# Performance work log

Measured on AMD Instinct MI355X. Metric: run time of the kernel, lower is better.

Reference implementation:

```python
import jax, jax.numpy as jnp
import numpy as np

# Model dims (see init_kwargs)
B, S, H = 1, 1024, 2048
NH, NKV, HD = 16, 4, 128       # query heads, kv heads (GQA), head dim
RD = 64                        # partial rotary dim
E, TOPK, I = 8, 2, 1024        # experts, top-k, expert intermediate
EPS = 1e-6
THETA = 1000000.0


def setup_inputs() -> dict:
    key = jax.random.key(0)
    ks = jax.random.split(key, 12)
    s = 0.02  # init scale
    return {
        "hidden_states": jax.random.normal(ks[0], (B, S, H), jnp.float32),
        "position_ids": jnp.tile(jnp.arange(S, dtype=jnp.int32), (B, 1)),
        "ln1_w": jnp.ones((H,), jnp.float32),
        "q_norm_w": jnp.ones((NH * HD,), jnp.float32),
        "k_norm_w": jnp.ones((NKV * HD,), jnp.float32),
        "wq": jax.random.normal(ks[1], (H, NH * HD), jnp.float32) * s,
        "wk": jax.random.normal(ks[2], (H, NKV * HD), jnp.float32) * s,
        "wv": jax.random.normal(ks[3], (H, NKV * HD), jnp.float32) * s,
        "wo": jax.random.normal(ks[4], (NH * HD, H), jnp.float32) * s,
        "ln2_w": jnp.ones((H,), jnp.float32),
        "router_w": jax.random.normal(ks[5], (H, E), jnp.float32) * s,
        "router_bias": jax.random.normal(ks[6], (E,), jnp.float32) * 0.1,
        "w_gate": jax.random.normal(ks[7], (E, H, I), jnp.float32) * s,
        "w_up": jax.random.normal(ks[8], (E, H, I), jnp.float32) * s,
        "w_down": jax.random.normal(ks[9], (E, I, H), jnp.float32) * s,
    }


def rmsnorm(x, w):
    # fp32 RMSNorm over full last dim (matches DistributedRMSNorm with tp=1)
    xf = x.astype(jnp.float32)
    r = jax.lax.rsqrt(jnp.mean(xf * xf, axis=-1, keepdims=True) + EPS)
    return (xf * r * w).astype(x.dtype)


def _rope(x, cos, sin):
    # partial rotary: only first RD dims of each head are rotated
    xr, xp = x[..., :RD], x[..., RD:]
    half = RD // 2
    rot = jnp.concatenate([-xr[..., half:], xr[..., :half]], axis=-1)
    return jnp.concatenate([xr * cos + rot * sin, xp], axis=-1)


def reference(hidden_states, position_ids, ln1_w, q_norm_w, k_norm_w,
              wq, wk, wv, wo, ln2_w, router_w, router_bias,
              w_gate, w_up, w_down):
    x = hidden_states
    # --- attention block ---
    h = rmsnorm(x, ln1_w)
    Q = h @ wq  # [B,S,NH*HD]
    K = h @ wk  # [B,S,NKV*HD]
    V = h @ wv
    # MiniMax M2 qk_norm: RMSNorm over FULL projection output BEFORE head reshape
    Q = rmsnorm(Q, q_norm_w)
    K = rmsnorm(K, k_norm_w)
    q = Q.reshape(B, S, NH, HD).transpose(0, 2, 1, 3)   # [B,NH,S,HD]
    k = K.reshape(B, S, NKV, HD).transpose(0, 2, 1, 3)  # [B,NKV,S,HD]
    v = V.reshape(B, S, NKV, HD).transpose(0, 2, 1, 3)
    # partial RoPE
    inv = 1.0 / (THETA ** (jnp.arange(0, RD, 2, dtype=jnp.float32) / RD))
    ang = position_ids.astype(jnp.float32)[:, :, None] * inv  # [B,S,RD/2]
    cos = jnp.concatenate([jnp.cos(ang)] * 2, axis=-1)[:, None]  # [B,1,S,RD]
    sin = jnp.concatenate([jnp.sin(ang)] * 2, axis=-1)[:, None]
    q = _rope(q, cos, sin)
    k = _rope(k, cos, sin)
    # GQA expand
    rep = NH // NKV
    k = jnp.repeat(k, rep, axis=1)
    v = jnp.repeat(v, rep, axis=1)
    scores = jnp.einsum('bhqd,bhkd->bhqk', q, k).astype(jnp.float32) / np.sqrt(HD).astype(np.float32)
    causal = jnp.tril(jnp.ones((S, S), bool))
    scores = jnp.where(causal, scores, jnp.float32(-1e30))
    attn = jax.nn.softmax(scores, axis=-1).astype(v.dtype)
    ctx = jnp.einsum('bhqk,bhkd->bhqd', attn, v)
    attn_out = ctx.transpose(0, 2, 1, 3).reshape(B, S, NH * HD) @ wo
    res = x + attn_out
    # --- MoE block ---
    h2 = rmsnorm(res, ln2_w)
    t = h2.reshape(B * S, H)
    logits = t.astype(jnp.float32) @ router_w        # [T,E]
    sc = jax.nn.sigmoid(logits)
    # top-k chosen on bias-corrected scores; weights from uncorrected scores
    _, ti = jax.lax.top_k(sc + router_bias, TOPK)    # [T,TOPK]
    aff = jnp.take_along_axis(sc, ti, axis=-1)
    aff = aff / jnp.sum(aff, axis=-1, keepdims=True)  # normalize_top_k_affinities
    T = B * S
    combine = jnp.zeros((T, E), jnp.float32).at[jnp.arange(T)[:, None], ti].add(aff)
    # SwiGLU experts (dense-compute, sparse-combine reference for blockwise grouped GEMM)
    g = jnp.einsum('th,ehi->tei', t, w_gate)
    u = jnp.einsum('th,ehi->tei', t, w_up)
    act = jax.nn.silu(g) * u
    eo = jnp.einsum('tei,eih->teh', act, w_down)
    moe = jnp.einsum('te,teh->th', combine.astype(eo.dtype), eo)
    return res + moe.reshape(B, S, H)
```

## Files before the change

### kernel.cpp

```cpp
#include <hip/hip_runtime.h>
#include <hip/hip_bf16.h>
#include <cstdint>

static constexpr int S   = 1024;
static constexpr int H   = 2048;
static constexpr int NH  = 16;
static constexpr int NKV = 4;
static constexpr int HD  = 128;
static constexpr int EXPN = 8;
static constexpr int FFI = 1024;

typedef __bf16 bf16x8 __attribute__((ext_vector_type(8)));
typedef float  f32x4  __attribute__((ext_vector_type(4)));
typedef unsigned short ushortx8 __attribute__((ext_vector_type(8)));

#define DEVI __device__ __forceinline__

DEVI unsigned short f2bf(float f) {
    union { float f; uint32_t u; } v; v.f = f;
    uint32_t r = (v.u + 0x7FFFu + ((v.u >> 16) & 1u)) >> 16;
    return (unsigned short)r;
}
DEVI float bf2f(unsigned short s) {
    union { uint32_t u; float f; } v; v.u = ((uint32_t)s) << 16; return v.f;
}

DEVI void atomAdd(float* p, float v) { unsafeAtomicAdd(p, v); }

DEVI void gll16(const unsigned short* g, unsigned short* l) {
    __builtin_amdgcn_global_load_lds(
        (const __attribute__((address_space(1))) unsigned int*)(g),
        (__attribute__((address_space(3))) unsigned int*)(l),
        16, 0, 0);
}

template<int N> DEVI void waitvm() {
    if constexpr (N == 0)      asm volatile("s_waitcnt vmcnt(0)" ::: "memory");
    else if constexpr (N == 2) asm volatile("s_waitcnt vmcnt(2)" ::: "memory");
    else if constexpr (N == 4) asm volatile("s_waitcnt vmcnt(4)" ::: "memory");
    else if constexpr (N == 6) asm volatile("s_waitcnt vmcnt(6)" ::: "memory");
    else static_assert(N == 0 || N == 2 || N == 4 || N == 6, "unsupported vmcnt");
}
DEVI void pipe_barrier() {
    __builtin_amdgcn_sched_barrier(0);
    __builtin_amdgcn_s_barrier();
    __builtin_amdgcn_sched_barrier(0);
}

__global__ __launch_bounds__(256) void transT(const float* __restrict__ in,
                                              unsigned short* __restrict__ outp,
                                              int R, int C)
{
    __shared__ unsigned short tl[64][72];
    int zb = blockIdx.z;
    in   += (size_t)zb * R * C;
    outp += (size_t)zb * R * C;
    int c0 = blockIdx.x * 64, r0 = blockIdx.y * 64;
    int t = threadIdx.x;
    int cq = (t & 15) * 4;
    int rr = t >> 4;
    #pragma unroll
    for (int p = 0; p < 4; ++p) {
        int row = rr + p * 16;
        float4 v = *(const float4*)&in[(size_t)(r0 + row) * C + c0 + cq];
        tl[cq + 0][row] = f2bf(v.x);
        tl[cq + 1][row] = f2bf(v.y);
        tl[cq + 2][row] = f2bf(v.z);
        tl[cq + 3][row] = f2bf(v.w);
    }
    __syncthreads();
    int r8 = (t & 7) * 8;
    int cc = t >> 3;
    #pragma unroll
    for (int p = 0; p < 2; ++p) {
        int col = cc + p * 32;
        ushortx8 v = *(const ushortx8*)&tl[col][r8];
        *(ushortx8*)&outp[(size_t)(c0 + col) * R + r0 + r8] = v;
    }
}

enum { CFG_PROJ3 = 0, CFG_WO = 1, CFG_SCORES = 2, CFG_PV = 3, CFG_GATEUP = 4, CFG_DOWN = 5 };

template<int CFG, int WM, int NI>
__global__ __launch_bounds__(256, 2) void gemm_k(
    const unsigned short* __restrict__ A,
    const unsigned short* __restrict__ B0,
    const unsigned short* __restrict__ B1,
    const unsigned short* __restrict__ B2,
    float* __restrict__ C0,
    float* __restrict__ C1,
    float* __restrict__ C2,
    unsigned short* __restrict__ Cb,
    const float* __restrict__ X,
    const int* __restrict__ cnt,
    const int* __restrict__ tokList,
    int arg0)
{
    constexpr bool DUAL = (CFG == CFG_GATEUP);
    constexpr int BM = WM * 32;
    constexpr int BN = NI * 32;
    constexpr int ASZ = BM * 64;
    constexpr int BSZ = BN * 64;
    constexpr int LD = WM + NI + (DUAL ? NI : 0);

    const int tid = threadIdx.x;
    const int m0 = blockIdx.y * BM;
    int n0 = blockIdx.x * BN;

    int M = S;
    int kbeg = 0, kend = 0, LDA = 0, LDBK = 0, LDC = 0;
    const unsigned short* Ap = A;
    const unsigned short* Bb = B0;
    const unsigned short* Bb2 = B1;
    const int* tlist = nullptr;
    float* Cout = C0;
    int head = 0, e = 0, hl = 0;

    if constexpr (CFG == CFG_PROJ3) {
        int xt = blockIdx.x;
        if (xt < 16)      { Bb = B0; Cout = C0; LDC = 2048; n0 = xt * 128; }
        else if (xt < 20) { Bb = B1; Cout = C1; LDC = 512;  n0 = (xt - 16) * 128; }
        else              { Bb = B2; Cout = C2; LDC = 512;  n0 = (xt - 20) * 128; }
        LDA = H; LDBK = H; kend = H;
    } else if constexpr (CFG == CFG_WO) {
        LDA = H; LDBK = H; LDC = H; kend = H;
    } else if constexpr (CFG == CFG_SCORES) {
        hl = blockIdx.z; head = arg0 + hl;
        if (n0 >= m0 + BM) return;
        Ap = A + (size_t)head * S * HD;
        Bb = B0 + (size_t)(head >> 2) * S * HD;
        kend = HD; LDA = HD; LDBK = HD;
    } else if constexpr (CFG == CFG_PV) {
        int z = blockIdx.z; hl = z >> 2; int ks = z & 3;
        head = arg0 + hl;
        int kcap = m0 + BM;
        kbeg = ks * 256;
        if (kbeg >= kcap) return;
        kend = (kbeg + 256 < kcap) ? kbeg + 256 : kcap;
        Ap = A + (size_t)hl * S * S;
        Bb = B0 + (size_t)(head >> 2) * HD * S;
        LDA = S; LDBK = S;
    } else if constexpr (CFG == CFG_GATEUP) {
        e = blockIdx.z;
        M = cnt[e]; if (m0 >= M) return;
        tlist = tokList + e * S;
        Bb  = B0 + (size_t)e * FFI * H;
        Bb2 = B1 + (size_t)e * FFI * H;
        kend = H; LDA = H; LDBK = H;
    } else {
        e = blockIdx.z;
        M = cnt[e]; if (m0 >= M) return;
        Ap = A + (size_t)e * S * FFI;
        Bb = B0 + (size_t)e * H * FFI;
        kend = FFI; LDA = FFI; LDBK = FFI;
    }

    __shared__ unsigned short As[3 * ASZ];
    __shared__ unsigned short Bs[3 * BSZ];
    __shared__ unsigned short Bs2[DUAL ? 3 * BSZ : 8];

    const int lane = tid & 63, grp = lane >> 4, r16 = lane & 15;
    const int wid = tid >> 6, wr = wid >> 1, wc = wid & 1;
    const int wbase8 = (tid & 0xFFC0) * 8;

    size_t aoff[WM];
    #pragma unroll
    for (int c = 0; c < WM; ++c) {
        int chunk = c * 256 + tid;
        int row = chunk >> 3;
        int kcs = (chunk & 7) * 8;
        int grow = m0 + row;
        if constexpr (CFG == CFG_GATEUP) { int r2 = grow < M ? grow : M - 1; grow = tlist[r2]; }
        else if constexpr (CFG == CFG_DOWN) { grow = grow < M ? grow : M - 1; }
        aoff[c] = (size_t)grow * LDA + (kcs ^ ((row & 7) << 3));
    }
    size_t boff[NI];
    #pragma unroll
    for (int c = 0; c < NI; ++c) {
        int chunk = c * 256 + tid;
        int row = chunk >> 3;
        int kcs = (chunk & 7) * 8;
        boff[c] = (size_t)(n0 + row) * LDBK + (kcs ^ ((row & 7) << 3));
    }

    auto STAGE = [&](int buf, int k0) {
        #pragma unroll
        for (int c = 0; c < WM; ++c)
            gll16(Ap + aoff[c] + k0, &As[buf * ASZ + c * 2048 + wbase8]);
        #pragma unroll
        for (int c = 0; c < NI; ++c)
            gll16(Bb + boff[c] + k0, &Bs[buf * BSZ + c * 2048 + wbase8]);
        if constexpr (DUAL) {
            #pragma unroll
            for (int c = 0; c < NI; ++c)
                gll16(Bb2 + boff[c] + k0, &Bs2[buf * BSZ + c * 2048 + wbase8]);
        }
    };

    f32x4 acc[WM][NI] = {};
    f32x4 acc2[DUAL ? WM : 1][DUAL ? NI : 1] = {};

    auto COMPUTE = [&](int buf) {
        #pragma unroll
        for (int kk = 0; kk < 64; kk += 32) {
            bf16x8 af[WM], bfr[NI], bfr2[DUAL ? NI : 1];
            #pragma unroll
            for (int mi = 0; mi < WM; ++mi) {
                int r = wr * (WM * 16) + mi * 16 + r16;
                int idx = buf * ASZ + r * 64 + ((kk + grp * 8) ^ ((r & 7) << 3));
                af[mi] = __builtin_bit_cast(bf16x8, *(const ushortx8*)&As[idx]);
            }
            #pragma unroll
            for (int ni = 0; ni < NI; ++ni) {
                int r = wc * (NI * 16) + ni * 16 + r16;
                int idx = buf * BSZ + r * 64 + ((kk + grp * 8) ^ ((r & 7) << 3));
                bfr[ni] = __builtin_bit_cast(bf16x8, *(const ushortx8*)&Bs[idx]);
                if constexpr (DUAL)
                    bfr2[ni] = __builtin_bit_cast(bf16x8, *(const ushortx8*)&Bs2[idx]);
            }
            #pragma unroll
            for (int mi = 0; mi < WM; ++mi)
                #pragma unroll
                for (int ni = 0; ni < NI; ++ni) {
                    acc[mi][ni] = __builtin_amdgcn_mfma_f32_16x16x32_bf16(af[mi], bfr[ni], acc[mi][ni], 0, 0, 0);
                    if constexpr (DUAL)
                        acc2[mi][ni] = __builtin_amdgcn_mfma_f32_16x16x32_bf16(af[mi], bfr2[ni], acc2[mi][ni], 0, 0, 0);
                }
        }
    };

    const int nk = (kend - kbeg) >> 6;

    STAGE(0, kbeg);
    if (nk > 1) STAGE(1, kbeg + 64);
    if (nk > 1) waitvm<LD>(); else waitvm<0>();
    pipe_barrier();

    int cur = 0, stg = 2;
    for (int i = 0; i < nk; ++i) {
        if (i + 2 < nk) {
            STAGE(stg, kbeg + (i + 2) * 64);
            stg = (stg == 2) ? 0 : stg + 1;
        }
        COMPUTE(cur);
        cur = (cur == 2) ? 0 : cur + 1;
        if (i + 1 < nk) {
            if (i + 2 < nk) waitvm<LD>();
            else            waitvm<0>();
            pipe_barrier();
        }
    }

    #pragma unroll
    for (int mi = 0; mi < WM; ++mi) {
        #pragma unroll
        for (int ni = 0; ni < NI; ++ni) {
            f32x4 v = acc[mi][ni];
            int col = n0 + wc * (NI * 16) + ni * 16 + r16;
            #pragma unroll
            for (int j = 0; j < 4; ++j) {
                int row = m0 + wr * (WM * 16) + mi * 16 + grp * 4 + j;
                float val = v[j];
                if constexpr (CFG == CFG_PROJ3) {
                    Cout[(size_t)row * LDC + col] = val;
                } else if constexpr (CFG == CFG_WO) {
                    C0[(size_t)row * H + col] = val + X[(size_t)row * H + col];
                } else if constexpr (CFG == CFG_SCORES) {
                    float sv = val * 0.08838834764831845f;
                    if (col > row) sv = -1e30f;
                    C0[((size_t)hl * S + row) * S + col] = sv;
                } else if constexpr (CFG == CFG_PV) {
                    atomAdd(&C0[(size_t)row * 2048 + head * HD + col], val);
                } else if constexpr (CFG == CFG_GATEUP) {
                    if (row < M) {
                        float g = val, u = acc2[mi][ni][j];
                        float a = g / (1.f + expf(-g)) * u;
                        Cb[((size_t)e * S + row) * FFI + col] = f2bf(a);
                    }
                } else {
                    if (row < M) {
                        Cb[((size_t)e * S + row) * H + col] = f2bf(val);
                    }
                }
            }
        }
    }
}

__global__ __launch_bounds__(256) void rms_h(const float* __restrict__ x,
                                             const float* __restrict__ w,
                                             unsigned short* __restrict__ out)
{
    int row = blockIdx.x, tid = threadIdx.x;
    const float* xr = x + (size_t)row * H;
    float4 a = *(const float4*)&xr[tid * 8];
    float4 b = *(const float4*)&xr[tid * 8 + 4];
    float vals[8] = { a.x, a.y, a.z, a.w, b.x, b.y, b.z, b.w };
    float ss = 0;
    #pragma unroll
    for (int j = 0; j < 8; ++j) ss += vals[j] * vals[j];
    __shared__ float red[4];
    #pragma unroll
    for (int o = 32; o; o >>= 1) ss += __shfl_down(ss, o);
    if ((tid & 63) == 0) red[tid >> 6] = ss;
    __syncthreads();
    float tot = red[0] + red[1] + red[2] + red[3];
    float r = rsqrtf(tot * (1.f / H) + 1e-6f);
    ushortx8 ov;
    #pragma unroll
    for (int j = 0; j < 8; ++j) ov[j] = f2bf(vals[j] * r * w[tid * 8 + j]);
    *(ushortx8*)&out[(size_t)row * H + tid * 8] = ov;
}

__global__ __launch_bounds__(256) void qnorm_rope(const float* __restrict__ qbuf,
                                                  const float* __restrict__ qw,
                                                  const int* __restrict__ pos,
                                                  unsigned short* __restrict__ qatt)
{
    int tok = blockIdx.x, tid = threadIdx.x;
    __shared__ float sh[2048];
    __shared__ float red[4];
    const float* xr = qbuf + (size_t)tok * 2048;
    float4 a = *(const float4*)&xr[tid * 8];
    float4 b = *(const float4*)&xr[tid * 8 + 4];
    *(float4*)&sh[tid * 8] = a;
    *(float4*)&sh[tid * 8 + 4] = b;
    float ss = a.x*a.x + a.y*a.y + a.z*a.z + a.w*a.w + b.x*b.x + b.y*b.y + b.z*b.z + b.w*b.w;
    #pragma unroll
    for (int o = 32; o; o >>= 1) ss += __shfl_down(ss, o);
    if ((tid & 63) == 0) red[tid >> 6] = ss;
    __syncthreads();
    float tot = red[0] + red[1] + red[2] + red[3];
    float r = rsqrtf(tot * (1.f / 2048.f) + 1e-6f);
    float p = (float)pos[tok];
    #pragma unroll
    for (int j = 0; j < 8; ++j) {
        int idx = tid * 8 + j;
        int d = idx & 127, hh = idx >> 7;
        float v = sh[idx] * r * qw[idx];
        float o;
        if (d < 64) {
            int jj = d & 31;
            float ang = p * expf((float)jj * -0.43173470268f);
            float c = cosf(ang), sn = sinf(ang);
            if (d < 32) { float v2 = sh[idx + 32] * r * qw[idx + 32]; o = v * c - v2 * sn; }
            else        { float v2 = sh[idx - 32] * r * qw[idx - 32]; o = v * c + v2 * sn; }
        } else o = v;
        qatt[((size_t)hh * S + tok) * HD + d] = f2bf(o);
    }
}

__global__ __launch_bounds__(256) void knorm_rope(const float* __restrict__ kbuf,
                                                  const float* __restrict__ kw,
                                                  const int* __restrict__ pos,
                                                  unsigned short* __restrict__ katt)
{
    int tok = blockIdx.x, tid = threadIdx.x;
    __shared__ float sh[512];
    __shared__ float red[4];
    const float* xr = kbuf + (size_t)tok * 512;
    float2 a = *(const float2*)&xr[tid * 2];
    sh[tid * 2] = a.x; sh[tid * 2 + 1] = a.y;
    float ss = a.x * a.x + a.y * a.y;
    #pragma unroll
    for (int o = 32; o; o >>= 1) ss += __shfl_down(ss, o);
    if ((tid & 63) == 0) red[tid >> 6] = ss;
    __syncthreads();
    float tot = red[0] + red[1] + red[2] + red[3];
    float r = rsqrtf(tot * (1.f / 512.f) + 1e-6f);
    float p = (float)pos[tok];
    #pragma unroll
    for (int j = 0; j < 2; ++j) {
        int idx = tid * 2 + j;
        int d = idx & 127, hh = idx >> 7;
        float v = sh[idx] * r * kw[idx];
        float o;
        if (d < 64) {
            int jj = d & 31;
            float ang = p * expf((float)jj * -0.43173470268f);
            float c = cosf(ang), sn = sinf(ang);
            if (d < 32) { float v2 = sh[idx + 32] * r * kw[idx + 32]; o = v * c - v2 * sn; }
            else        { float v2 = sh[idx - 32] * r * kw[idx - 32]; o = v * c + v2 * sn; }
        } else o = v;
        katt[((size_t)hh * S + tok) * HD + d] = f2bf(o);
    }
}

__global__ __launch_bounds__(256) void softmax_k(const float* __restrict__ scores,
                                                 unsigned short* __restrict__ pb)
{
    int bid = blockIdx.x;
    int hl = bid >> 10, q = bid & 1023;
    const float* srow = scores + ((size_t)hl * S + q) * S;
    unsigned short* prow = pb + ((size_t)hl * S + q) * S;
    int L = q + 1, tid = threadIdx.x;
    __shared__ float red[4];
    float v[4]; float mx = -3.4e38f;
    #pragma unroll
    for (int i = 0; i < 4; ++i) {
        int j = tid + i * 256;
        if (j < L) { v[i] = srow[j]; mx = fmaxf(mx, v[i]); } else v[i] = 0.f;
    }
    float m = mx;
    #pragma unroll
    for (int o = 32; o; o >>= 1) m = fmaxf(m, __shfl_down(m, o));
    if ((tid & 63) == 0) red[tid >> 6] = m;
    __syncthreads();
    float M_ = fmaxf(fmaxf(red[0], red[1]), fmaxf(red[2], red[3]));
    __syncthreads();
    float e[4]; float sum = 0;
    #pragma unroll
    for (int i = 0; i < 4; ++i) {
        int j = tid + i * 256;
        if (j < L) { e[i] = expf(v[i] - M_); sum += e[i]; } else e[i] = 0.f;
    }
    #pragma unroll
    for (int o = 32; o; o >>= 1) sum += __shfl_down(sum, o);
    if ((tid & 63) == 0) red[tid >> 6] = sum;
    __syncthreads();
    float inv = 1.f / (red[0] + red[1] + red[2] + red[3]);
    #pragma unroll
    for (int i = 0; i < 4; ++i) {
        int j = tid + i * 256;
        prow[j] = f2bf(e[i] * inv);
    }
}

__global__ void zero_cnt(int* cnt) { if (threadIdx.x < EXPN) cnt[threadIdx.x] = 0; }

__global__ void zerok(float4* __restrict__ p, int n4)
{
    int i = blockIdx.x * 256 + threadIdx.x;
    if (i < n4) p[i] = float4{0.f, 0.f, 0.f, 0.f};
}

__global__ void cvt_k(const float* __restrict__ src, unsigned short* __restrict__ dst)
{
    int i = blockIdx.x * 256 + threadIdx.x;
    float4 a = *(const float4*)&src[i * 8];
    float4 b = *(const float4*)&src[i * 8 + 4];
    float v[8] = { a.x, a.y, a.z, a.w, b.x, b.y, b.z, b.w };
    ushortx8 o;
    #pragma unroll
    for (int j = 0; j < 8; ++j) o[j] = f2bf(v[j]);
    *(ushortx8*)&dst[i * 8] = o;
}

__global__ __launch_bounds__(256) void router_k(const float* __restrict__ res,
                                                const float* __restrict__ ln2w,
                                                const float* __restrict__ rw,
                                                const float* __restrict__ rbias,
                                                int* __restrict__ cnt,
                                                int* __restrict__ tokList,
                                                int* __restrict__ slot,
                                                float* __restrict__ slotw)
{
    int tok = blockIdx.x, tid = threadIdx.x;
    const float* xr = res + (size_t)tok * H;
    float4 a = *(const float4*)&xr[tid * 8];
    float4 b = *(const float4*)&xr[tid * 8 + 4];
    float vals[8] = { a.x, a.y, a.z, a.w, b.x, b.y, b.z, b.w };
    float ss = 0;
    #pragma unroll
    for (int j = 0; j < 8; ++j) ss += vals[j] * vals[j];
    __shared__ float red[4];
    float t_ = ss;
    #pragma unroll
    for (int o = 32; o; o >>= 1) t_ += __shfl_down(t_, o);
    if ((tid & 63) == 0) red[tid >> 6] = t_;
    __syncthreads();
    float tot = red[0] + red[1] + red[2] + red[3];
    float r = rsqrtf(tot * (1.f / H) + 1e-6f);

    float acc[EXPN] = {};
    #pragma unroll
    for (int j = 0; j < 8; ++j) {
        float tv = vals[j] * r * ln2w[tid * 8 + j];
        const float* rp = rw + (size_t)(tid * 8 + j) * EXPN;
        #pragma unroll
        for (int e = 0; e < EXPN; ++e) acc[e] += tv * rp[e];
    }
    __shared__ float r8[4][EXPN];
    #pragma unroll
    for (int e = 0; e < EXPN; ++e) {
        float s_ = acc[e];
        #pragma unroll
        for (int o = 32; o; o >>= 1) s_ += __shfl_down(s_, o);
        acc[e] = s_;
    }
    if ((tid & 63) == 0)
        for (int e = 0; e < EXPN; ++e) r8[tid >> 6][e] = acc[e];
    __syncthreads();
    if (tid == 0) {
        float sg[EXPN];
        for (int e = 0; e < EXPN; ++e) {
            float lg = r8[0][e] + r8[1][e] + r8[2][e] + r8[3][e];
            sg[e] = 1.f / (1.f + expf(-lg));
        }
        int i0 = 0; float b0 = -1e30f;
        for (int e = 0; e < EXPN; ++e) {
            float s_ = sg[e] + rbias[e];
            if (s_ > b0) { b0 = s_; i0 = e; }
        }
        int i1 = -1; float b1 = -1e30f;
        for (int e = 0; e < EXPN; ++e) {
            if (e == i0) continue;
            float s_ = sg[e] + rbias[e];
            if (s_ > b1) { b1 = s_; i1 = e; }
        }
        float a0 = sg[i0], a1 = sg[i1], inv = 1.f / (a0 + a1);
        int p0 = atomicAdd(&cnt[i0], 1);
        tokList[i0 * S + p0] = tok;
        int p1 = atomicAdd(&cnt[i1], 1);
        tokList[i1 * S + p1] = tok;
        slot[tok * 2]     = i0 * S + p0;  slotw[tok * 2]     = a0 * inv;
        slot[tok * 2 + 1] = i1 * S + p1;  slotw[tok * 2 + 1] = a1 * inv;
    }
}

__global__ __launch_bounds__(256) void combine_k(const unsigned short* __restrict__ eo,
                                                 const int* __restrict__ slot,
                                                 const float* __restrict__ slotw,
                                                 float* __restrict__ out)
{
    int t = blockIdx.x;
    int c = threadIdx.x * 8;
    int s0 = slot[t * 2], s1 = slot[t * 2 + 1];
    float w0 = slotw[t * 2], w1 = slotw[t * 2 + 1];
    ushortx8 a = *(const ushortx8*)&eo[(size_t)s0 * H + c];
    ushortx8 b = *(const ushortx8*)&eo[(size_t)s1 * H + c];
    size_t base = (size_t)t * H + c;
    float4 o0 = *(float4*)&out[base];
    float4 o1 = *(float4*)&out[base + 4];
    float ov[8] = { o0.x, o0.y, o0.z, o0.w, o1.x, o1.y, o1.z, o1.w };
    #pragma unroll
    for (int j = 0; j < 8; ++j)
        ov[j] += w0 * bf2f(a[j]) + w1 * bf2f(b[j]);
    *(float4*)&out[base]     = float4{ ov[0], ov[1], ov[2], ov[3] };
    *(float4*)&out[base + 4] = float4{ ov[4], ov[5], ov[6], ov[7] };
}

extern "C" void kernel_launch(void* const* d_in, const int* in_sizes, int n_in,
                              void* d_out, int out_size, void* d_ws, size_t ws_size,
                              hipStream_t stream)
{
    const float* x     = (const float*)d_in[0];
    const int*   pos   = (const int*)d_in[1];
    const float* ln1w  = (const float*)d_in[2];
    const float* qnw   = (const float*)d_in[3];
    const float* knw   = (const float*)d_in[4];
    const float* wq    = (const float*)d_in[5];
    const float* wk    = (const float*)d_in[6];
    const float* wv    = (const float*)d_in[7];
    const float* wo    = (const float*)d_in[8];
    const float* ln2w  = (const float*)d_in[9];
    const float* rw    = (const float*)d_in[10];
    const float* rbias = (const float*)d_in[11];
    const float* wg    = (const float*)d_in[12];
    const float* wu    = (const float*)d_in[13];
    const float* wd    = (const float*)d_in[14];
    float* out = (float*)d_out;

    char* ws = (char*)d_ws;
    const size_t MB = 1024 * 1024;
    unsigned short* h_bf = (unsigned short*)(ws + 0);
    float* qbuf  = (float*)(ws + 4 * MB);
    float* ctxf  = (float*)(ws + 4 * MB);
    float* kbuf  = (float*)(ws + 12 * MB);
    float* vbuf  = (float*)(ws + 14 * MB);
    unsigned short* qatt = (unsigned short*)(ws + 16 * MB);
    unsigned short* katt = (unsigned short*)(ws + 20 * MB);
    unsigned short* vT   = (unsigned short*)(ws + 21 * MB);
    unsigned short* ctx  = (unsigned short*)(ws + 22 * MB);
    unsigned short* tbf  = (unsigned short*)(ws + 26 * MB);
    int*   cnt     = (int*)(ws + 30 * MB);
    int*   tokList = (int*)(ws + 30 * MB + 4096);
    int*   slot    = (int*)(ws + 30 * MB + 512 * 1024);
    float* slotw   = (float*)(ws + 30 * MB + 768 * 1024);
    float* scores = (float*)(ws + 31 * MB);
    unsigned short* pbuf = (unsigned short*)(ws + 63 * MB);
    unsigned short* act = (unsigned short*)(ws + 31 * MB);
    unsigned short* eo  = (unsigned short*)(ws + 47 * MB);
    unsigned short* wqT = (unsigned short*)(ws + 79 * MB);
    unsigned short* wkT = (unsigned short*)(ws + 87 * MB);
    unsigned short* wvT = (unsigned short*)(ws + 89 * MB);
    unsigned short* woT = (unsigned short*)(ws + 91 * MB);
    unsigned short* wgT = (unsigned short*)(ws + 99 * MB);
    unsigned short* wuT = (unsigned short*)(ws + 131 * MB);
    unsigned short* wdT = (unsigned short*)(ws + 163 * MB);

    transT<<<dim3(32, 32, 1), 256, 0, stream>>>(wq, wqT, 2048, 2048);
    transT<<<dim3(8,  32, 1), 256, 0, stream>>>(wk, wkT, 2048, 512);
    transT<<<dim3(8,  32, 1), 256, 0, stream>>>(wv, wvT, 2048, 512);
    transT<<<dim3(32, 32, 1), 256, 0, stream>>>(wo, woT, 2048, 2048);
    transT<<<dim3(16, 32, 8), 256, 0, stream>>>(wg, wgT, 2048, 1024);
    transT<<<dim3(16, 32, 8), 256, 0, stream>>>(wu, wuT, 2048, 1024);
    transT<<<dim3(32, 16, 8), 256, 0, stream>>>(wd, wdT, 1024, 2048);

    rms_h<<<S, 256, 0, stream>>>(x, ln1w, h_bf);

    gemm_k<CFG_PROJ3, 2, 4><<<dim3(24, 16, 1), 256, 0, stream>>>(h_bf, wqT, wkT, wvT, qbuf, kbuf, vbuf, nullptr, nullptr, nullptr, nullptr, 0);

    qnorm_rope<<<S, 256, 0, stream>>>(qbuf, qnw, pos, qatt);
    knorm_rope<<<S, 256, 0, stream>>>(kbuf, knw, pos, katt);
    transT<<<dim3(8, 16, 1), 256, 0, stream>>>(vbuf, vT, 1024, 512);
    zerok<<<2048, 256, 0, stream>>>((float4*)ctxf, (8 * MB) / 16);

    for (int hc = 0; hc < 2; ++hc) {
        gemm_k<CFG_SCORES, 2, 4><<<dim3(8, 16, 8), 256, 0, stream>>>(qatt, katt, nullptr, nullptr, scores, nullptr, nullptr, nullptr, nullptr, nullptr, nullptr, hc * 8);
        softmax_k<<<8 * S, 256, 0, stream>>>(scores, pbuf);
        gemm_k<CFG_PV, 2, 4><<<dim3(1, 16, 32), 256, 0, stream>>>(pbuf, vT, nullptr, nullptr, ctxf, nullptr, nullptr, nullptr, nullptr, nullptr, nullptr, hc * 8);
    }
    cvt_k<<<(S * 2048) / (256 * 8), 256, 0, stream>>>(ctxf, ctx);

    gemm_k<CFG_WO, 2, 4><<<dim3(16, 16, 1), 256, 0, stream>>>(ctx, woT, nullptr, nullptr, out, nullptr, nullptr, nullptr, x, nullptr, nullptr, 0);

    rms_h<<<S, 256, 0, stream>>>(out, ln2w, tbf);
    zero_cnt<<<1, 64, 0, stream>>>(cnt);
    router_k<<<S, 256, 0, stream>>>(out, ln2w, rw, rbias, cnt, tokList, slot, slotw);

    gemm_k<CFG_GATEUP, 2, 2><<<dim3(16, 16, EXPN), 256, 0, stream>>>(tbf, wgT, wuT, nullptr, nullptr, nullptr, nullptr, act, nullptr, cnt, tokList, 0);
    gemm_k<CFG_DOWN, 2, 2><<<dim3(32, 16, EXPN), 256, 0, stream>>>(act, wdT, nullptr, nullptr, nullptr, nullptr, nullptr, eo, nullptr, cnt, tokList, 0);
    combine_k<<<S, 256, 0, stream>>>(eo, slot, slotw, out);
}
```

Before: 383.7 us.

## Store attention scores in bf16 in place, batch all heads, retune GEMM tiles

The scores GEMM now writes bf16 scores instead of fp32, and softmax overwrites them in place with vectorized 4-wide loads and stores. This removes the separate fp32 score buffer and the probability buffer, so all 16 heads run in one launch instead of two chunks. The GEMM gains a PIPE template flag that picks between a 3-stage pipeline and a simpler 2-buffer loop with syncthreads, chosen per call site. PROJ3 and WO switch to narrower tiles with twice as many blocks. Rounding scores to bf16 before softmax loses some precision in the logits.

Result: faster. 335.3 us (-12.6%).

```diff
diff --git a/kernel.cpp b/kernel.cpp
--- a/kernel.cpp
+++ b/kernel.cpp
@@ -13,6 +13,7 @@
 typedef __bf16 bf16x8 __attribute__((ext_vector_type(8)));
 typedef float  f32x4  __attribute__((ext_vector_type(4)));
 typedef unsigned short ushortx8 __attribute__((ext_vector_type(8)));
+typedef unsigned short ushortx4 __attribute__((ext_vector_type(4)));
 
 #define DEVI __device__ __forceinline__
 
@@ -81,7 +82,7 @@
 
 enum { CFG_PROJ3 = 0, CFG_WO = 1, CFG_SCORES = 2, CFG_PV = 3, CFG_GATEUP = 4, CFG_DOWN = 5 };
 
-template<int CFG, int WM, int NI>
+template<int CFG, int WM, int NI, bool PIPE>
 __global__ __launch_bounds__(256, 2) void gemm_k(
     const unsigned short* __restrict__ A,
     const unsigned short* __restrict__ B0,
@@ -101,6 +102,7 @@
     constexpr int BN = NI * 32;
     constexpr int ASZ = BM * 64;
     constexpr int BSZ = BN * 64;
+    constexpr int NBUF = PIPE ? 3 : 2;
     constexpr int LD = WM + NI + (DUAL ? NI : 0);
 
     const int tid = threadIdx.x;
@@ -118,9 +120,9 @@
 
     if constexpr (CFG == CFG_PROJ3) {
         int xt = blockIdx.x;
-        if (xt < 16)      { Bb = B0; Cout = C0; LDC = 2048; n0 = xt * 128; }
-        else if (xt < 20) { Bb = B1; Cout = C1; LDC = 512;  n0 = (xt - 16) * 128; }
-        else              { Bb = B2; Cout = C2; LDC = 512;  n0 = (xt - 20) * 128; }
+        if (xt < 32)      { Bb = B0; Cout = C0; LDC = 2048; n0 = xt * 64; }
+        else if (xt < 40) { Bb = B1; Cout = C1; LDC = 512;  n0 = (xt - 32) * 64; }
+        else              { Bb = B2; Cout = C2; LDC = 512;  n0 = (xt - 40) * 64; }
         LDA = H; LDBK = H; kend = H;
     } else if constexpr (CFG == CFG_WO) {
         LDA = H; LDBK = H; LDC = H; kend = H;
@@ -155,9 +157,9 @@
         kend = FFI; LDA = FFI; LDBK = FFI;
     }
 
-    __shared__ unsigned short As[3 * ASZ];
-    __shared__ unsigned short Bs[3 * BSZ];
-    __shared__ unsigned short Bs2[DUAL ? 3 * BSZ : 8];
+    __shared__ unsigned short As[NBUF * ASZ];
+    __shared__ unsigned short Bs[NBUF * BSZ];
+    __shared__ unsigned short Bs2[DUAL ? NBUF * BSZ : 8];
 
     const int lane = tid & 63, grp = lane >> 4, r16 = lane & 15;
     const int wid = tid >> 6, wr = wid >> 1, wc = wid & 1;
@@ -229,25 +231,35 @@
         }
     };
 
-    const int nk = (kend - kbeg) >> 6;
-
-    STAGE(0, kbeg);
-    if (nk > 1) STAGE(1, kbeg + 64);
-    if (nk > 1) waitvm<LD>(); else waitvm<0>();
-    pipe_barrier();
-
-    int cur = 0, stg = 2;
-    for (int i = 0; i < nk; ++i) {
-        if (i + 2 < nk) {
-            STAGE(stg, kbeg + (i + 2) * 64);
-            stg = (stg == 2) ? 0 : stg + 1;
-        }
-        COMPUTE(cur);
-        cur = (cur == 2) ? 0 : cur + 1;
-        if (i + 1 < nk) {
-            if (i + 2 < nk) waitvm<LD>();
-            else            waitvm<0>();
-            pipe_barrier();
+    if constexpr (PIPE) {
+        const int nk = (kend - kbeg) >> 6;
+        STAGE(0, kbeg);
+        if (nk > 1) STAGE(1, kbeg + 64);
+        if (nk > 1) waitvm<LD>(); else waitvm<0>();
+        pipe_barrier();
+        int cur = 0, stg = 2;
+        for (int i = 0; i < nk; ++i) {
+            if (i + 2 < nk) {
+                STAGE(stg, kbeg + (i + 2) * 64);
+                stg = (stg == 2) ? 0 : stg + 1;
+            }
+            COMPUTE(cur);
+            cur = (cur == 2) ? 0 : cur + 1;
+            if (i + 1 < nk) {
+                if (i + 2 < nk) waitvm<LD>();
+                else            waitvm<0>();
+                pipe_barrier();
+            }
+        }
+    } else {
+        int cur = 0;
+        STAGE(0, kbeg);
+        __syncthreads();
+        for (int k0 = kbeg; k0 < kend; k0 += 64) {
+            if (k0 + 64 < kend) STAGE(cur ^ 1, k0 + 64);
+            COMPUTE(cur);
+            __syncthreads();
+            cur ^= 1;
         }
     }
 
@@ -268,7 +280,7 @@
                 } else if constexpr (CFG == CFG_SCORES) {
                     float sv = val * 0.08838834764831845f;
                     if (col > row) sv = -1e30f;
-                    C0[((size_t)hl * S + row) * S + col] = sv;
+                    Cb[((size_t)hl * S + row) * S + col] = f2bf(sv);
                 } else if constexpr (CFG == CFG_PV) {
                     atomAdd(&C0[(size_t)row * 2048 + head * HD + col], val);
                 } else if constexpr (CFG == CFG_GATEUP) {
@@ -386,20 +398,20 @@
     }
 }
 
-__global__ __launch_bounds__(256) void softmax_k(const float* __restrict__ scores,
-                                                 unsigned short* __restrict__ pb)
+__global__ __launch_bounds__(256) void softmax_k(unsigned short* __restrict__ sc)
 {
     int bid = blockIdx.x;
     int hl = bid >> 10, q = bid & 1023;
-    const float* srow = scores + ((size_t)hl * S + q) * S;
-    unsigned short* prow = pb + ((size_t)hl * S + q) * S;
+    unsigned short* srow = sc + ((size_t)hl * S + q) * S;
     int L = q + 1, tid = threadIdx.x;
     __shared__ float red[4];
+    ushortx4 in4 = *(const ushortx4*)&srow[tid * 4];
     float v[4]; float mx = -3.4e38f;
     #pragma unroll
     for (int i = 0; i < 4; ++i) {
-        int j = tid + i * 256;
-        if (j < L) { v[i] = srow[j]; mx = fmaxf(mx, v[i]); } else v[i] = 0.f;
+        int j = tid * 4 + i;
+        if (j < L) { v[i] = bf2f(in4[i]); mx = fmaxf(mx, v[i]); }
+        else v[i] = -3.4e38f;
     }
     float m = mx;
     #pragma unroll
@@ -411,7 +423,7 @@
     float e[4]; float sum = 0;
     #pragma unroll
     for (int i = 0; i < 4; ++i) {
-        int j = tid + i * 256;
+        int j = tid * 4 + i;
         if (j < L) { e[i] = expf(v[i] - M_); sum += e[i]; } else e[i] = 0.f;
     }
     #pragma unroll
@@ -419,11 +431,10 @@
     if ((tid & 63) == 0) red[tid >> 6] = sum;
     __syncthreads();
     float inv = 1.f / (red[0] + red[1] + red[2] + red[3]);
-    #pragma unroll
-    for (int i = 0; i < 4; ++i) {
-        int j = tid + i * 256;
-        prow[j] = f2bf(e[i] * inv);
-    }
+    ushortx4 o4;
+    #pragma unroll
+    for (int i = 0; i < 4; ++i) o4[i] = f2bf(e[i] * inv);
+    *(ushortx4*)&srow[tid * 4] = o4;
 }
 
 __global__ void zero_cnt(int* cnt) { if (threadIdx.x < EXPN) cnt[threadIdx.x] = 0; }
@@ -577,8 +588,7 @@
     int*   tokList = (int*)(ws + 30 * MB + 4096);
     int*   slot    = (int*)(ws + 30 * MB + 512 * 1024);
     float* slotw   = (float*)(ws + 30 * MB + 768 * 1024);
-    float* scores = (float*)(ws + 31 * MB);
-    unsigned short* pbuf = (unsigned short*)(ws + 63 * MB);
+    unsigned short* scores = (unsigned short*)(ws + 31 * MB);
     unsigned short* act = (unsigned short*)(ws + 31 * MB);
     unsigned short* eo  = (unsigned short*)(ws + 47 * MB);
     unsigned short* wqT = (unsigned short*)(ws + 79 * MB);
@@ -599,27 +609,25 @@
 
     rms_h<<<S, 256, 0, stream>>>(x, ln1w, h_bf);
 
-    gemm_k<CFG_PROJ3, 2, 4><<<dim3(24, 16, 1), 256, 0, stream>>>(h_bf, wqT, wkT, wvT, qbuf, kbuf, vbuf, nullptr, nullptr, nullptr, nullptr, 0);
+    gemm_k<CFG_PROJ3, 2, 2, true><<<dim3(48, 16, 1), 256, 0, stream>>>(h_bf, wqT, wkT, wvT, qbuf, kbuf, vbuf, nullptr, nullptr, nullptr, nullptr, 0);
 
     qnorm_rope<<<S, 256, 0, stream>>>(qbuf, qnw, pos, qatt);
     knorm_rope<<<S, 256, 0, stream>>>(kbuf, knw, pos, katt);
     transT<<<dim3(8, 16, 1), 256, 0, stream>>>(vbuf, vT, 1024, 512);
     zerok<<<2048, 256, 0, stream>>>((float4*)ctxf, (8 * MB) / 16);
 
-    for (int hc = 0; hc < 2; ++hc) {
-        gemm_k<CFG_SCORES, 2, 4><<<dim3(8, 16, 8), 256, 0, stream>>>(qatt, katt, nullptr, nullptr, scores, nullptr, nullptr, nullptr, nullptr, nullptr, nullptr, hc * 8);
-        softmax_k<<<8 * S, 256, 0, stream>>>(scores, pbuf);
-        gemm_k<CFG_PV, 2, 4><<<dim3(1, 16, 32), 256, 0, stream>>>(pbuf, vT, nullptr, nullptr, ctxf, nullptr, nullptr, nullptr, nullptr, nullptr, nullptr, hc * 8);
-    }
+    gemm_k<CFG_SCORES, 2, 4, false><<<dim3(8, 16, 16), 256, 0, stream>>>(qatt, katt, nullptr, nullptr, nullptr, nullptr, nullptr, scores, nullptr, nullptr, nullptr, 0);
+    softmax_k<<<16 * S, 256, 0, stream>>>(scores);
+    gemm_k<CFG_PV, 2, 4, false><<<dim3(1, 16, 64), 256, 0, stream>>>(scores, vT, nullptr, nullptr, ctxf, nullptr, nullptr, nullptr, nullptr, nullptr, nullptr, 0);
     cvt_k<<<(S * 2048) / (256 * 8), 256, 0, stream>>>(ctxf, ctx);
 
-    gemm_k<CFG_WO, 2, 4><<<dim3(16, 16, 1), 256, 0, stream>>>(ctx, woT, nullptr, nullptr, out, nullptr, nullptr, nullptr, x, nullptr, nullptr, 0);
+    gemm_k<CFG_WO, 2, 2, true><<<dim3(32, 16, 1), 256, 0, stream>>>(ctx, woT, nullptr, nullptr, out, nullptr, nullptr, nullptr, x, nullptr, nullptr, 0);
 
     rms_h<<<S, 256, 0, stream>>>(out, ln2w, tbf);
     zero_cnt<<<1, 64, 0, stream>>>(cnt);
     router_k<<<S, 256, 0, stream>>>(out, ln2w, rw, rbias, cnt, tokList, slot, slotw);
 
-    gemm_k<CFG_GATEUP, 2, 2><<<dim3(16, 16, EXPN), 256, 0, stream>>>(tbf, wgT, wuT, nullptr, nullptr, nullptr, nullptr, act, nullptr, cnt, tokList, 0);
-    gemm_k<CFG_DOWN, 2, 2><<<dim3(32, 16, EXPN), 256, 0, stream>>>(act, wdT, nullptr, nullptr, nullptr, nullptr, nullptr, eo, nullptr, cnt, tokList, 0);
+    gemm_k<CFG_GATEUP, 2, 2, false><<<dim3(16, 16, EXPN), 256, 0, stream>>>(tbf, wgT, wuT, nullptr, nullptr, nullptr, nullptr, act, nullptr, cnt, tokList, 0);
+    gemm_k<CFG_DOWN, 2, 2, true><<<dim3(32, 16, EXPN), 256, 0, stream>>>(act, wdT, nullptr, nullptr, nullptr, nullptr, nullptr, eo, nullptr, cnt, tokList, 0);
     combine_k<<<S, 256, 0, stream>>>(eo, slot, slotw, out);
 }
```
